# Kernel tuning notes

Measured on AMD Instinct MI355X. Metric: run time of the kernel, lower is better.

The kernel has to match this reference:

```python
import jax, jax.numpy as jnp
import numpy as np

D_MODEL = 768
NUM_HEADS = 12
HEAD_DIM = D_MODEL // NUM_HEADS


def setup_inputs() -> dict:
    key = jax.random.key(0)
    ks = jax.random.split(key, 9)
    B, S = 2, 2048
    s = 1.0 / np.sqrt(D_MODEL)
    x = jax.random.normal(ks[0], (B, S, D_MODEL), dtype=jnp.float32)
    Wq = jax.random.normal(ks[1], (D_MODEL, D_MODEL), dtype=jnp.float32) * s
    Wk = jax.random.normal(ks[2], (D_MODEL, D_MODEL), dtype=jnp.float32) * s
    Wv = jax.random.normal(ks[3], (D_MODEL, D_MODEL), dtype=jnp.float32) * s
    Wo = jax.random.normal(ks[4], (D_MODEL, D_MODEL), dtype=jnp.float32) * s
    bq = jax.random.normal(ks[5], (D_MODEL,), dtype=jnp.float32) * 0.01
    bk = jax.random.normal(ks[6], (D_MODEL,), dtype=jnp.float32) * 0.01
    bv = jax.random.normal(ks[7], (D_MODEL,), dtype=jnp.float32) * 0.01
    bo = jax.random.normal(ks[8], (D_MODEL,), dtype=jnp.float32) * 0.01
    return {"x": x, "Wq": Wq, "bq": bq, "Wk": Wk, "bk": bk,
            "Wv": Wv, "bv": bv, "Wo": Wo, "bo": bo}


def reference(x, Wq, bq, Wk, bk, Wv, bv, Wo, bo):
    B, S, _ = x.shape
    # projections; reshape to [B, H, S, Dh]
    def split_heads(t):
        return t.reshape(B, S, NUM_HEADS, HEAD_DIM).transpose(0, 2, 1, 3)
    q = split_heads(x @ Wq + bq)
    k = split_heads(x @ Wk + bk)
    v = split_heads(x @ Wv + bv)
    scale = 1.0 / np.sqrt(HEAD_DIM)
    scores = jnp.einsum("bhqd,bhkd->bhqk", q, k) * scale  # [B,H,S,S]
    attn = jax.nn.softmax(scores, axis=-1)
    # dropout p=0.0 (eval) -> identity
    ctx = jnp.einsum("bhqk,bhkd->bhqd", attn, v)
    ctx = ctx.transpose(0, 2, 1, 3).reshape(B, S, D_MODEL)
    return ctx @ Wo + bo
```

## Files before the change

kernel.cpp:

```cpp
#include <hip/hip_runtime.h>
#include <hip/hip_bf16.h>
#include <hip/hip_fp16.h>

#define D_MODEL 768
#define NHEADS  12
#define HD      64
#define BATCH   2
#define SEQ     2048
#define NTOK    (BATCH*SEQ)
#define NX      ((size_t)NTOK * D_MODEL)
#define NW      ((size_t)D_MODEL * D_MODEL)
#define SC_LOG2 0.18033688f

typedef __attribute__((ext_vector_type(8))) short    short8;
typedef __attribute__((ext_vector_type(8))) _Float16 half8;
typedef __attribute__((ext_vector_type(2))) __fp16   fp16x2;
typedef __attribute__((ext_vector_type(4))) float    f32x4;

__device__ __forceinline__ float bf2f(short s) {
    union { unsigned u; float f; } c;
    c.u = ((unsigned)(unsigned short)s) << 16;
    return c.f;
}
__device__ __forceinline__ short f2bf(float f) {
    __hip_bfloat16 h = __float2bfloat16(f);
    return *(short*)&h;
}

#ifdef __has_builtin
#if __has_builtin(__builtin_amdgcn_global_load_lds)
#define HAS_GLD 1
#endif
#if __has_builtin(__builtin_amdgcn_exp2f)
#define EXP2(x) __builtin_amdgcn_exp2f(x)
#else
#define EXP2(x) exp2f(x)
#endif
#if __has_builtin(__builtin_amdgcn_cvt_pkrtz)
#define HAS_PKRTZ 1
#endif
#else
#define EXP2(x) exp2f(x)
#endif
#ifdef HAS_GLD
#define GLD16(gp, lp) __builtin_amdgcn_global_load_lds( \
    (const __attribute__((address_space(1))) void*)(gp), \
    (__attribute__((address_space(3))) void*)(lp), 16, 0, 0)
#endif

__global__ __launch_bounds__(256) void fused_conv(
        const void* __restrict__ xin,
        const void* __restrict__ w0, const void* __restrict__ w1,
        const void* __restrict__ w2, const void* __restrict__ w3,
        const void* __restrict__ b0, const void* __restrict__ b1,
        const void* __restrict__ b2, const void* __restrict__ b3,
        short* __restrict__ xc, short* __restrict__ wt,
        short* __restrict__ bc, int* __restrict__ flag)
{
    __shared__ int red[256];
    __shared__ float T[64][65];
    const int tid = threadIdx.x;
    const int F = blockIdx.x;

    {
        const short* xs = (const short*)xin;
        int maxe = 0;
#pragma unroll
        for (int u = 0; u < 16; ++u) {
            int e = ((unsigned short)xs[tid * 16 + u] >> 7) & 0xFF;
            maxe = max(maxe, e);
        }
        red[tid] = maxe;
        __syncthreads();
        for (int s = 128; s > 0; s >>= 1) {
            if (tid < s) red[tid] = max(red[tid], red[tid + s]);
            __syncthreads();
        }
    }
    const bool isf = (red[0] > 140);

    if (F < 3072) {
        const int i = F * 256 + tid;
        if (isf) {
            float4 f = ((const float4*)xin)[i];
            short4 o = { f2bf(f.x), f2bf(f.y), f2bf(f.z), f2bf(f.w) };
            ((short4*)xc)[i] = o;
        } else {
            ((short4*)xc)[i] = ((const short4*)xin)[i];
        }
    } else if (F < 3648) {
        const int G = F - 3072;
        const int z = G / 144, rr = G % 144;
        const int k0 = (rr % 12) * 64, n0 = (rr / 12) * 64;
        const void* src = (z == 0) ? w0 : (z == 1) ? w1 : (z == 2) ? w2 : w3;
        const float sc = (z == 0) ? SC_LOG2 : 1.0f;
        const int la = tid & 15, lb = tid >> 4;
#pragma unroll
        for (int u = 0; u < 4; ++u) {
            const int kr = (lb & 3) + 4 * u + 16 * (lb >> 2);
            if (isf) {
                float4 f = *(const float4*)((const float*)src + (size_t)(k0 + kr) * D_MODEL + n0 + la * 4);
                T[kr][la*4+0] = f.x; T[kr][la*4+1] = f.y; T[kr][la*4+2] = f.z; T[kr][la*4+3] = f.w;
            } else {
                short4 s = *(const short4*)((const short*)src + (size_t)(k0 + kr) * D_MODEL + n0 + la * 4);
                T[kr][la*4+0] = bf2f(s.x); T[kr][la*4+1] = bf2f(s.y);
                T[kr][la*4+2] = bf2f(s.z); T[kr][la*4+3] = bf2f(s.w);
            }
        }
        __syncthreads();
#pragma unroll
        for (int u = 0; u < 4; ++u) {
            const int nr = (lb & 3) + 4 * u + 16 * (lb >> 2);
            short4 o = { f2bf(T[la*4+0][nr] * sc), f2bf(T[la*4+1][nr] * sc),
                         f2bf(T[la*4+2][nr] * sc), f2bf(T[la*4+3][nr] * sc) };
            *(short4*)(wt + (size_t)z * NW + (size_t)(n0 + nr) * D_MODEL + k0 + la * 4) = o;
        }
    } else {
        if (tid == 0) *flag = isf ? 1 : 0;
        const void* srcs[4] = { b0, b1, b2, b3 };
        for (int z = 0; z < 4; ++z) {
            const float sc = (z == 0) ? SC_LOG2 : 1.0f;
            for (int i = tid; i < D_MODEL; i += 256) {
                float v = isf ? ((const float*)srcs[z])[i] : bf2f(((const short*)srcs[z])[i]);
                bc[z * D_MODEL + i] = f2bf(v * sc);
            }
        }
    }
}

__global__ __launch_bounds__(256) void qkv_gemm(const short* __restrict__ X,
                                                const short* __restrict__ Wt,
                                                const short* __restrict__ bias,
                                                short* __restrict__ qb,
                                                short* __restrict__ kb,
                                                _Float16* __restrict__ Vt)
{
    __shared__ __align__(16) char shbuf[32768];
    short* Als = (short*)shbuf;
    short* Bls = (short*)(shbuf + 16384);
    _Float16* T = (_Float16*)shbuf;

    const int tid = threadIdx.x;
    const int wave = tid >> 6, lane = tid & 63;
    const int quad = lane >> 4, l16 = lane & 15;
    const int wm = wave & 1, wn = wave >> 1;
    const int m0 = blockIdx.x * 128;
    const int ng = blockIdx.y * 128;

    f32x4 acc[4][4];
#pragma unroll
    for (int nt = 0; nt < 4; ++nt) {
        const float bv = bf2f(bias[ng + wn*64 + nt*16 + l16]);
#pragma unroll
        for (int mt = 0; mt < 4; ++mt) acc[mt][nt] = (f32x4){bv, bv, bv, bv};
    }

    const int row = tid >> 2, ch = (tid & 3) * 8;
#ifdef HAS_GLD
#define QSTAGE(buf, k0) do { \
        GLD16(X  + (size_t)(m0 + row)      * D_MODEL + (k0) + ch, &Als[(buf)*4096 + tid*8]); \
        GLD16(X  + (size_t)(m0 + 64 + row) * D_MODEL + (k0) + ch, &Als[(buf)*4096 + 2048 + tid*8]); \
        GLD16(Wt + (size_t)(ng + row)      * D_MODEL + (k0) + ch, &Bls[(buf)*4096 + tid*8]); \
        GLD16(Wt + (size_t)(ng + 64 + row) * D_MODEL + (k0) + ch, &Bls[(buf)*4096 + 2048 + tid*8]); \
    } while (0)
#else
#define QSTAGE(buf, k0) do { \
        short8 r0 = *(const short8*)(X  + (size_t)(m0 + row)      * D_MODEL + (k0) + ch); \
        short8 r1 = *(const short8*)(X  + (size_t)(m0 + 64 + row) * D_MODEL + (k0) + ch); \
        short8 r2 = *(const short8*)(Wt + (size_t)(ng + row)      * D_MODEL + (k0) + ch); \
        short8 r3 = *(const short8*)(Wt + (size_t)(ng + 64 + row) * D_MODEL + (k0) + ch); \
        *(short8*)&Als[(buf)*4096 + tid*8] = r0;  *(short8*)&Als[(buf)*4096 + 2048 + tid*8] = r1; \
        *(short8*)&Bls[(buf)*4096 + tid*8] = r2;  *(short8*)&Bls[(buf)*4096 + 2048 + tid*8] = r3; \
    } while (0)
#endif

    QSTAGE(0, 0);
    __syncthreads();

    for (int ks = 0; ks < 24; ++ks) {
        const int cur = ks & 1;
        if (ks + 1 < 24) QSTAGE(cur ^ 1, (ks + 1) * 32);

        short8 a[4], b[4];
#pragma unroll
        for (int mt = 0; mt < 4; ++mt)
            a[mt] = *(const short8*)&Als[cur*4096 + (wm*64 + mt*16 + l16) * 32 + quad*8];
#pragma unroll
        for (int nt = 0; nt < 4; ++nt)
            b[nt] = *(const short8*)&Bls[cur*4096 + (wn*64 + nt*16 + l16) * 32 + quad*8];
#pragma unroll
        for (int mt = 0; mt < 4; ++mt)
#pragma unroll
        for (int nt = 0; nt < 4; ++nt)
            acc[mt][nt] = __builtin_amdgcn_mfma_f32_16x16x32_bf16(a[mt], b[nt], acc[mt][nt], 0, 0, 0);

        __syncthreads();
    }
#undef QSTAGE

    const int seg = blockIdx.y / 6;
    if (seg < 2) {
        short* out = seg ? kb : qb;
        const int nl = ng - seg * 768;
#pragma unroll
        for (int mt = 0; mt < 4; ++mt)
#pragma unroll
        for (int nt = 0; nt < 4; ++nt) {
            const int n = nl + wn*64 + nt*16 + l16;
#pragma unroll
            for (int r = 0; r < 4; ++r) {
                const int m = m0 + wm*64 + mt*16 + quad*4 + r;
                out[(size_t)m * D_MODEL + n] = f2bf(acc[mt][nt][r]);
            }
        }
    } else {
        const int batch = m0 >> 11, tokb = m0 & (SEQ - 1);
        for (int pass = 0; pass < 2; ++pass) {
            if (wn == pass) {
#pragma unroll
                for (int nt = 0; nt < 4; ++nt) {
                    const int dim_l = nt*16 + l16;
#pragma unroll
                    for (int mt = 0; mt < 4; ++mt) {
                        const int tok_l = wm*64 + mt*16 + quad*4;
                        union { _Float16 h4[4]; int2 v; } u;
#pragma unroll
                        for (int r = 0; r < 4; ++r) u.h4[r] = (_Float16)acc[mt][nt][r];
                        *(int2*)&T[dim_l * 136 + tok_l] = u.v;
                    }
                }
            }
            __syncthreads();
#pragma unroll
            for (int u = 0; u < 4; ++u) {
                const int slot = tid + u * 256;
                const int drow = slot >> 4, chk = slot & 15;
                int4 val = *(const int4*)&T[drow * 136 + chk * 8];
                const int dim_g = ng - 1536 + pass*64 + drow;
                const int h = dim_g >> 6, d = dim_g & 63;
                *(int4*)(Vt + ((size_t)(batch * NHEADS + h) * HD + d) * SEQ + tokb + chk*8) = val;
            }
            if (pass == 0) __syncthreads();
        }
    }
}

__global__ __launch_bounds__(256) void out_gemm(const short* __restrict__ X,
                                                const short* __restrict__ Wt,
                                                const short* __restrict__ bias,
                                                void* __restrict__ outv,
                                                const int* __restrict__ flag)
{
    __shared__ short Als[2][2048];
    __shared__ short Bls[2][2048];

    const int tid = threadIdx.x;
    const int wave = tid >> 6, lane = tid & 63;
    const int quad = lane >> 4, l16 = lane & 15;
    const int m0 = blockIdx.x * 64;
    const int n0 = blockIdx.y * 64;

    f32x4 acc[4];
#pragma unroll
    for (int nt = 0; nt < 4; ++nt) {
        const float bv = bf2f(bias[n0 + nt*16 + l16]);
        acc[nt] = (f32x4){bv, bv, bv, bv};
    }

    const int row = tid >> 2, ch = (tid & 3) * 8;
#ifdef HAS_GLD
#define OSTAGE(buf, k0) do { \
        GLD16(X  + (size_t)(m0 + row) * D_MODEL + (k0) + ch, &Als[buf][tid*8]); \
        GLD16(Wt + (size_t)(n0 + row) * D_MODEL + (k0) + ch, &Bls[buf][tid*8]); \
    } while (0)
#else
#define OSTAGE(buf, k0) do { \
        short8 r0 = *(const short8*)(X  + (size_t)(m0 + row) * D_MODEL + (k0) + ch); \
        short8 r1 = *(const short8*)(Wt + (size_t)(n0 + row) * D_MODEL + (k0) + ch); \
        *(short8*)&Als[buf][tid*8] = r0; \
        *(short8*)&Bls[buf][tid*8] = r1; \
    } while (0)
#endif

    OSTAGE(0, 0);
    __syncthreads();

    for (int ks = 0; ks < 24; ++ks) {
        const int cur = ks & 1;
        if (ks + 1 < 24) OSTAGE(cur ^ 1, (ks + 1) * 32);

        short8 a = *(const short8*)&Als[cur][(wave*16 + l16) * 32 + quad*8];
#pragma unroll
        for (int nt = 0; nt < 4; ++nt) {
            short8 b = *(const short8*)&Bls[cur][(nt*16 + l16) * 32 + quad*8];
            acc[nt] = __builtin_amdgcn_mfma_f32_16x16x32_bf16(a, b, acc[nt], 0, 0, 0);
        }
        __syncthreads();
    }
#undef OSTAGE

    const bool outf32 = (*flag != 0);
#pragma unroll
    for (int nt = 0; nt < 4; ++nt) {
        const int n = n0 + nt*16 + l16;
#pragma unroll
        for (int r = 0; r < 4; ++r) {
            const int m = m0 + wave*16 + quad*4 + r;
            const size_t idx = (size_t)m * D_MODEL + n;
            if (outf32) ((float*)outv)[idx] = acc[nt][r];
            else        ((short*)outv)[idx] = f2bf(acc[nt][r]);
        }
    }
}

__global__ __launch_bounds__(256) void attn_mfma(const short* __restrict__ q,
                                                 const short* __restrict__ k,
                                                 const _Float16* __restrict__ Vt,
                                                 short* __restrict__ ctx)
{
    __shared__ short    Kls[2][64 * 64];
    __shared__ _Float16 Vls[2][64 * 64];
    __shared__ _Float16 Pls[4][16 * 64];

    const int tid  = threadIdx.x;
    const int wave = tid >> 6, lane = tid & 63;
    const int quad = lane >> 4, l16 = lane & 15;

    const int F = blockIdx.x;
    const int xcd = F & 7, slot = F >> 3;
    const int bh = xcd * 3 + (slot >> 5);
    const int q0 = (slot & 31) * 64;
    const int b = bh / NHEADS, h = bh % NHEADS;
    const size_t bS = (size_t)b * SEQ;
    const int myq = q0 + wave * 16 + l16;

    short8 qf[2];
#pragma unroll
    for (int k0h = 0; k0h < 2; ++k0h)
        qf[k0h] = *(const short8*)(q + (bS + myq) * D_MODEL + h*HD + k0h*32 + quad*8);

    half8 ones;
#pragma unroll
    for (int j = 0; j < 8; ++j) ones[j] = (_Float16)1.0f;

    const int s0 = tid, s1 = tid + 256;
    const int kr0 = s0 >> 3, kc0 = (s0 & 7) ^ (kr0 & 7);
    const int kr1 = s1 >> 3, kc1 = (s1 & 7) ^ (kr1 & 7);
    const short*    kg0 = k  + (bS + kr0) * D_MODEL + h*HD + kc0*8;
    const short*    kg1 = k  + (bS + kr1) * D_MODEL + h*HD + kc1*8;
    const _Float16* vg0 = Vt + ((size_t)bh * HD + kr0) * SEQ + kc0*8;
    const _Float16* vg1 = Vt + ((size_t)bh * HD + kr1) * SEQ + kc1*8;

#ifdef HAS_GLD
#define STAGE(buf, j0) do { \
        GLD16(kg0 + (size_t)(j0) * D_MODEL, &Kls[buf][s0 * 8]); \
        GLD16(kg1 + (size_t)(j0) * D_MODEL, &Kls[buf][s1 * 8]); \
        GLD16(vg0 + (j0),                   &Vls[buf][s0 * 8]); \
        GLD16(vg1 + (j0),                   &Vls[buf][s1 * 8]); \
    } while (0)
#else
#define STAGE(buf, j0) do { \
        short8 a_ = *(const short8*)(kg0 + (size_t)(j0) * D_MODEL); \
        short8 b_ = *(const short8*)(kg1 + (size_t)(j0) * D_MODEL); \
        half8  c_ = *(const half8*)(vg0 + (j0)); \
        half8  d_ = *(const half8*)(vg1 + (j0)); \
        *(short8*)&Kls[buf][s0 * 8] = a_;  *(short8*)&Kls[buf][s1 * 8] = b_; \
        *(half8*)&Vls[buf][s0 * 8] = c_;   *(half8*)&Vls[buf][s1 * 8] = d_; \
    } while (0)
#endif

    float m_ = -1e30f;
    f32x4 lacc = (f32x4){0.f, 0.f, 0.f, 0.f};
    f32x4 o[4];
#pragma unroll
    for (int t = 0; t < 4; ++t) o[t] = (f32x4){0.f, 0.f, 0.f, 0.f};

    STAGE(0, 0);
    __syncthreads();

    for (int jt = 0; jt < SEQ / 64; ++jt) {
        const int cur = jt & 1;
        if (jt + 1 < SEQ / 64) STAGE(cur ^ 1, (jt + 1) * 64);

        f32x4 s4[4];
#pragma unroll
        for (int t = 0; t < 4; ++t) s4[t] = (f32x4){0.f, 0.f, 0.f, 0.f};
#pragma unroll
        for (int k0h = 0; k0h < 2; ++k0h)
#pragma unroll
        for (int t = 0; t < 4; ++t) {
            const int krow = t*16 + l16;
            short8 kf = *(const short8*)&Kls[cur][krow*64 + (((k0h*4 + quad) ^ (krow & 7)) * 8)];
            s4[t] = __builtin_amdgcn_mfma_f32_16x16x32_bf16(kf, qf[k0h], s4[t], 0, 0, 0);
        }

        float mx = s4[0][0];
#pragma unroll
        for (int t = 0; t < 4; ++t)
#pragma unroll
        for (int r = 0; r < 4; ++r) mx = fmaxf(mx, s4[t][r]);
        if (__any(mx > m_)) {
#pragma unroll
            for (int d = 1; d < 64; d <<= 1) mx = fmaxf(mx, __shfl_xor(mx, d));
            const float mn = fmaxf(m_, mx);
            const float al = EXP2(m_ - mn);
#pragma unroll
            for (int t = 0; t < 4; ++t) {
                o[t][0] *= al; o[t][1] *= al; o[t][2] *= al; o[t][3] *= al;
            }
            lacc[0] *= al; lacc[1] *= al; lacc[2] *= al; lacc[3] *= al;
            m_ = mn;
        }

#pragma unroll
        for (int t = 0; t < 4; ++t) {
            union { fp16x2 h2[2]; int2 v; } u4;
#ifdef HAS_PKRTZ
            u4.h2[0] = __builtin_amdgcn_cvt_pkrtz(EXP2(s4[t][0] - m_), EXP2(s4[t][1] - m_));
            u4.h2[1] = __builtin_amdgcn_cvt_pkrtz(EXP2(s4[t][2] - m_), EXP2(s4[t][3] - m_));
#else
            u4.h2[0] = (fp16x2){ (__fp16)EXP2(s4[t][0] - m_), (__fp16)EXP2(s4[t][1] - m_) };
            u4.h2[1] = (fp16x2){ (__fp16)EXP2(s4[t][2] - m_), (__fp16)EXP2(s4[t][3] - m_) };
#endif
            const int c = (t*2 + (quad >> 1)) ^ (l16 & 7);
            *(int2*)&Pls[wave][l16*64 + c*8 + (quad & 1)*4] = u4.v;
        }

#pragma unroll
        for (int k0h = 0; k0h < 2; ++k0h) {
            const int pc = (k0h*4 + quad) ^ (l16 & 7);
            half8 pf = *(half8*)&Pls[wave][l16*64 + pc*8];
            lacc = __builtin_amdgcn_mfma_f32_16x16x32_f16(ones, pf, lacc, 0, 0, 0);
#pragma unroll
            for (int t = 0; t < 4; ++t) {
                const int vrow = t*16 + l16;
                half8 vf = *(const half8*)&Vls[cur][vrow*64 + (((k0h*4 + quad) ^ (vrow & 7)) * 8)];
                o[t] = __builtin_amdgcn_mfma_f32_16x16x32_f16(vf, pf, o[t], 0, 0, 0);
            }
        }

        __syncthreads();
    }

    const float inv = 1.0f / lacc[0];
    const size_t rowp = (bS + myq) * D_MODEL + h*HD;
#pragma unroll
    for (int t = 0; t < 4; ++t) {
        union { short s4v[4]; int2 v; } u4;
#pragma unroll
        for (int r = 0; r < 4; ++r) u4.s4v[r] = f2bf(o[t][r] * inv);
        *(int2*)(ctx + rowp + t*16 + quad*4) = u4.v;
    }
#undef STAGE
}

extern "C" void kernel_launch(void* const* d_in, const int* in_sizes, int n_in,
                              void* d_out, int out_size, void* d_ws, size_t ws_size,
                              hipStream_t stream)
{
    int* flag = (int*)d_ws;
    short* xc = (short*)((char*)d_ws + 64);
    short* Wt = xc + NX;
    short* bc = Wt + 4 * NW;
    short* qb = bc + 4 * D_MODEL;
    short* kb = qb + NX;
    _Float16* Vt = (_Float16*)(kb + NX);
    short* cb = (short*)(Vt + NX);

    fused_conv<<<3649, 256, 0, stream>>>(d_in[0],
                                         d_in[1], d_in[3], d_in[5], d_in[7],
                                         d_in[2], d_in[4], d_in[6], d_in[8],
                                         xc, Wt, bc, flag);

    qkv_gemm<<<dim3(NTOK/128, 2304/128), 256, 0, stream>>>(xc, Wt, bc, qb, kb, Vt);

    attn_mfma<<<768, 256, 0, stream>>>(qb, kb, Vt, cb);

    out_gemm<<<dim3(NTOK/64, D_MODEL/64), 256, 0, stream>>>(cb, Wt + 3*NW, bc + 3*D_MODEL, d_out, flag);
}
```

Baseline: 182.4 us.

## Process two 16-row query groups per wave in attention, halving block threads

```diff
diff --git a/kernel.cpp b/kernel.cpp
--- a/kernel.cpp
+++ b/kernel.cpp
@@ -313,14 +313,14 @@
     }
 }
 
-__global__ __launch_bounds__(256) void attn_mfma(const short* __restrict__ q,
+__global__ __launch_bounds__(128) void attn_mfma(const short* __restrict__ q,
                                                  const short* __restrict__ k,
                                                  const _Float16* __restrict__ Vt,
                                                  short* __restrict__ ctx)
 {
     __shared__ short    Kls[2][64 * 64];
     __shared__ _Float16 Vls[2][64 * 64];
-    __shared__ _Float16 Pls[4][16 * 64];
+    __shared__ _Float16 Pls[2][32 * 64];
 
     const int tid  = threadIdx.x;
     const int wave = tid >> 6, lane = tid & 63;
@@ -332,48 +332,77 @@
     const int q0 = (slot & 31) * 64;
     const int b = bh / NHEADS, h = bh % NHEADS;
     const size_t bS = (size_t)b * SEQ;
-    const int myq = q0 + wave * 16 + l16;
-
-    short8 qf[2];
+    const int qbase = q0 + wave * 32;
+
+    short8 qf[2][2];
+#pragma unroll
+    for (int qg = 0; qg < 2; ++qg)
 #pragma unroll
     for (int k0h = 0; k0h < 2; ++k0h)
-        qf[k0h] = *(const short8*)(q + (bS + myq) * D_MODEL + h*HD + k0h*32 + quad*8);
+        qf[qg][k0h] = *(const short8*)(q + (bS + qbase + qg*16 + l16) * D_MODEL
+                                         + h*HD + k0h*32 + quad*8);
 
     half8 ones;
 #pragma unroll
     for (int j = 0; j < 8; ++j) ones[j] = (_Float16)1.0f;
 
-    const int s0 = tid, s1 = tid + 256;
-    const int kr0 = s0 >> 3, kc0 = (s0 & 7) ^ (kr0 & 7);
-    const int kr1 = s1 >> 3, kc1 = (s1 & 7) ^ (kr1 & 7);
-    const short*    kg0 = k  + (bS + kr0) * D_MODEL + h*HD + kc0*8;
-    const short*    kg1 = k  + (bS + kr1) * D_MODEL + h*HD + kc1*8;
-    const _Float16* vg0 = Vt + ((size_t)bh * HD + kr0) * SEQ + kc0*8;
-    const _Float16* vg1 = Vt + ((size_t)bh * HD + kr1) * SEQ + kc1*8;
+    int kr[4], kc[4];
+#pragma unroll
+    for (int u = 0; u < 4; ++u) {
+        const int s = tid + u * 128;
+        kr[u] = s >> 3;
+        kc[u] = (s & 7) ^ (kr[u] & 7);
+    }
+    const short*    kg0 = k  + (bS + kr[0]) * D_MODEL + h*HD + kc[0]*8;
+    const short*    kg1 = k  + (bS + kr[1]) * D_MODEL + h*HD + kc[1]*8;
+    const short*    kg2 = k  + (bS + kr[2]) * D_MODEL + h*HD + kc[2]*8;
+    const short*    kg3 = k  + (bS + kr[3]) * D_MODEL + h*HD + kc[3]*8;
+    const _Float16* vg0 = Vt + ((size_t)bh * HD + kr[0]) * SEQ + kc[0]*8;
+    const _Float16* vg1 = Vt + ((size_t)bh * HD + kr[1]) * SEQ + kc[1]*8;
+    const _Float16* vg2 = Vt + ((size_t)bh * HD + kr[2]) * SEQ + kc[2]*8;
+    const _Float16* vg3 = Vt + ((size_t)bh * HD + kr[3]) * SEQ + kc[3]*8;
 
 #ifdef HAS_GLD
 #define STAGE(buf, j0) do { \
-        GLD16(kg0 + (size_t)(j0) * D_MODEL, &Kls[buf][s0 * 8]); \
-        GLD16(kg1 + (size_t)(j0) * D_MODEL, &Kls[buf][s1 * 8]); \
-        GLD16(vg0 + (j0),                   &Vls[buf][s0 * 8]); \
-        GLD16(vg1 + (j0),                   &Vls[buf][s1 * 8]); \
+        GLD16(kg0 + (size_t)(j0) * D_MODEL, &Kls[buf][(tid      ) * 8]); \
+        GLD16(kg1 + (size_t)(j0) * D_MODEL, &Kls[buf][(tid + 128) * 8]); \
+        GLD16(kg2 + (size_t)(j0) * D_MODEL, &Kls[buf][(tid + 256) * 8]); \
+        GLD16(kg3 + (size_t)(j0) * D_MODEL, &Kls[buf][(tid + 384) * 8]); \
+        GLD16(vg0 + (j0),                   &Vls[buf][(tid      ) * 8]); \
+        GLD16(vg1 + (j0),                   &Vls[buf][(tid + 128) * 8]); \
+        GLD16(vg2 + (j0),                   &Vls[buf][(tid + 256) * 8]); \
+        GLD16(vg3 + (j0),                   &Vls[buf][(tid + 384) * 8]); \
     } while (0)
 #else
 #define STAGE(buf, j0) do { \
-        short8 a_ = *(const short8*)(kg0 + (size_t)(j0) * D_MODEL); \
-        short8 b_ = *(const short8*)(kg1 + (size_t)(j0) * D_MODEL); \
-        half8  c_ = *(const half8*)(vg0 + (j0)); \
-        half8  d_ = *(const half8*)(vg1 + (j0)); \
-        *(short8*)&Kls[buf][s0 * 8] = a_;  *(short8*)&Kls[buf][s1 * 8] = b_; \
-        *(half8*)&Vls[buf][s0 * 8] = c_;   *(half8*)&Vls[buf][s1 * 8] = d_; \
+        short8 a0_ = *(const short8*)(kg0 + (size_t)(j0) * D_MODEL); \
+        short8 a1_ = *(const short8*)(kg1 + (size_t)(j0) * D_MODEL); \
+        short8 a2_ = *(const short8*)(kg2 + (size_t)(j0) * D_MODEL); \
+        short8 a3_ = *(const short8*)(kg3 + (size_t)(j0) * D_MODEL); \
+        half8  c0_ = *(const half8*)(vg0 + (j0)); \
+        half8  c1_ = *(const half8*)(vg1 + (j0)); \
+        half8  c2_ = *(const half8*)(vg2 + (j0)); \
+        half8  c3_ = *(const half8*)(vg3 + (j0)); \
+        *(short8*)&Kls[buf][(tid      ) * 8] = a0_; \
+        *(short8*)&Kls[buf][(tid + 128) * 8] = a1_; \
+        *(short8*)&Kls[buf][(tid + 256) * 8] = a2_; \
+        *(short8*)&Kls[buf][(tid + 384) * 8] = a3_; \
+        *(half8*)&Vls[buf][(tid      ) * 8] = c0_; \
+        *(half8*)&Vls[buf][(tid + 128) * 8] = c1_; \
+        *(half8*)&Vls[buf][(tid + 256) * 8] = c2_; \
+        *(half8*)&Vls[buf][(tid + 384) * 8] = c3_; \
     } while (0)
 #endif
 
     float m_ = -1e30f;
-    f32x4 lacc = (f32x4){0.f, 0.f, 0.f, 0.f};
-    f32x4 o[4];
-#pragma unroll
-    for (int t = 0; t < 4; ++t) o[t] = (f32x4){0.f, 0.f, 0.f, 0.f};
+    f32x4 lacc[2];
+    f32x4 o[2][4];
+#pragma unroll
+    for (int qg = 0; qg < 2; ++qg) {
+        lacc[qg] = (f32x4){0.f, 0.f, 0.f, 0.f};
+#pragma unroll
+        for (int t = 0; t < 4; ++t) o[qg][t] = (f32x4){0.f, 0.f, 0.f, 0.f};
+    }
 
     STAGE(0, 0);
     __syncthreads();
@@ -382,74 +411,96 @@
         const int cur = jt & 1;
         if (jt + 1 < SEQ / 64) STAGE(cur ^ 1, (jt + 1) * 64);
 
-        f32x4 s4[4];
-#pragma unroll
-        for (int t = 0; t < 4; ++t) s4[t] = (f32x4){0.f, 0.f, 0.f, 0.f};
+        f32x4 s4[2][4];
+#pragma unroll
+        for (int qg = 0; qg < 2; ++qg)
+#pragma unroll
+        for (int t = 0; t < 4; ++t) s4[qg][t] = (f32x4){0.f, 0.f, 0.f, 0.f};
 #pragma unroll
         for (int k0h = 0; k0h < 2; ++k0h)
 #pragma unroll
         for (int t = 0; t < 4; ++t) {
             const int krow = t*16 + l16;
             short8 kf = *(const short8*)&Kls[cur][krow*64 + (((k0h*4 + quad) ^ (krow & 7)) * 8)];
-            s4[t] = __builtin_amdgcn_mfma_f32_16x16x32_bf16(kf, qf[k0h], s4[t], 0, 0, 0);
-        }
-
-        float mx = s4[0][0];
+#pragma unroll
+            for (int qg = 0; qg < 2; ++qg)
+                s4[qg][t] = __builtin_amdgcn_mfma_f32_16x16x32_bf16(kf, qf[qg][k0h], s4[qg][t], 0, 0, 0);
+        }
+
+        float mx = s4[0][0][0];
+#pragma unroll
+        for (int qg = 0; qg < 2; ++qg)
 #pragma unroll
         for (int t = 0; t < 4; ++t)
 #pragma unroll
-        for (int r = 0; r < 4; ++r) mx = fmaxf(mx, s4[t][r]);
+        for (int r = 0; r < 4; ++r) mx = fmaxf(mx, s4[qg][t][r]);
         if (__any(mx > m_)) {
 #pragma unroll
             for (int d = 1; d < 64; d <<= 1) mx = fmaxf(mx, __shfl_xor(mx, d));
             const float mn = fmaxf(m_, mx);
             const float al = EXP2(m_ - mn);
 #pragma unroll
-            for (int t = 0; t < 4; ++t) {
-                o[t][0] *= al; o[t][1] *= al; o[t][2] *= al; o[t][3] *= al;
-            }
-            lacc[0] *= al; lacc[1] *= al; lacc[2] *= al; lacc[3] *= al;
+            for (int qg = 0; qg < 2; ++qg) {
+#pragma unroll
+                for (int t = 0; t < 4; ++t) {
+                    o[qg][t][0] *= al; o[qg][t][1] *= al;
+                    o[qg][t][2] *= al; o[qg][t][3] *= al;
+                }
+                lacc[qg][0] *= al; lacc[qg][1] *= al;
+                lacc[qg][2] *= al; lacc[qg][3] *= al;
+            }
             m_ = mn;
         }
 
+#pragma unroll
+        for (int qg = 0; qg < 2; ++qg)
 #pragma unroll
         for (int t = 0; t < 4; ++t) {
             union { fp16x2 h2[2]; int2 v; } u4;
 #ifdef HAS_PKRTZ
-            u4.h2[0] = __builtin_amdgcn_cvt_pkrtz(EXP2(s4[t][0] - m_), EXP2(s4[t][1] - m_));
-            u4.h2[1] = __builtin_amdgcn_cvt_pkrtz(EXP2(s4[t][2] - m_), EXP2(s4[t][3] - m_));
+            u4.h2[0] = __builtin_amdgcn_cvt_pkrtz(EXP2(s4[qg][t][0] - m_), EXP2(s4[qg][t][1] - m_));
+            u4.h2[1] = __builtin_amdgcn_cvt_pkrtz(EXP2(s4[qg][t][2] - m_), EXP2(s4[qg][t][3] - m_));
 #else
-            u4.h2[0] = (fp16x2){ (__fp16)EXP2(s4[t][0] - m_), (__fp16)EXP2(s4[t][1] - m_) };
-            u4.h2[1] = (fp16x2){ (__fp16)EXP2(s4[t][2] - m_), (__fp16)EXP2(s4[t][3] - m_) };
+            u4.h2[0] = (fp16x2){ (__fp16)EXP2(s4[qg][t][0] - m_), (__fp16)EXP2(s4[qg][t][1] - m_) };
+            u4.h2[1] = (fp16x2){ (__fp16)EXP2(s4[qg][t][2] - m_), (__fp16)EXP2(s4[qg][t][3] - m_) };
 #endif
             const int c = (t*2 + (quad >> 1)) ^ (l16 & 7);
-            *(int2*)&Pls[wave][l16*64 + c*8 + (quad & 1)*4] = u4.v;
+            *(int2*)&Pls[wave][(qg*16 + l16)*64 + c*8 + (quad & 1)*4] = u4.v;
         }
 
 #pragma unroll
         for (int k0h = 0; k0h < 2; ++k0h) {
             const int pc = (k0h*4 + quad) ^ (l16 & 7);
-            half8 pf = *(half8*)&Pls[wave][l16*64 + pc*8];
-            lacc = __builtin_amdgcn_mfma_f32_16x16x32_f16(ones, pf, lacc, 0, 0, 0);
+            half8 pf[2];
+#pragma unroll
+            for (int qg = 0; qg < 2; ++qg) {
+                pf[qg] = *(half8*)&Pls[wave][(qg*16 + l16)*64 + pc*8];
+                lacc[qg] = __builtin_amdgcn_mfma_f32_16x16x32_f16(ones, pf[qg], lacc[qg], 0, 0, 0);
+            }
 #pragma unroll
             for (int t = 0; t < 4; ++t) {
                 const int vrow = t*16 + l16;
                 half8 vf = *(const half8*)&Vls[cur][vrow*64 + (((k0h*4 + quad) ^ (vrow & 7)) * 8)];
-                o[t] = __builtin_amdgcn_mfma_f32_16x16x32_f16(vf, pf, o[t], 0, 0, 0);
+#pragma unroll
+                for (int qg = 0; qg < 2; ++qg)
+                    o[qg][t] = __builtin_amdgcn_mfma_f32_16x16x32_f16(vf, pf[qg], o[qg][t], 0, 0, 0);
             }
         }
 
         __syncthreads();
     }
 
-    const float inv = 1.0f / lacc[0];
-    const size_t rowp = (bS + myq) * D_MODEL + h*HD;
-#pragma unroll
-    for (int t = 0; t < 4; ++t) {
-        union { short s4v[4]; int2 v; } u4;
-#pragma unroll
-        for (int r = 0; r < 4; ++r) u4.s4v[r] = f2bf(o[t][r] * inv);
-        *(int2*)(ctx + rowp + t*16 + quad*4) = u4.v;
+#pragma unroll
+    for (int qg = 0; qg < 2; ++qg) {
+        const float inv = 1.0f / lacc[qg][0];
+        const size_t rowp = (bS + qbase + qg*16 + l16) * D_MODEL + h*HD;
+#pragma unroll
+        for (int t = 0; t < 4; ++t) {
+            union { short s4v[4]; int2 v; } u4;
+#pragma unroll
+            for (int r = 0; r < 4; ++r) u4.s4v[r] = f2bf(o[qg][t][r] * inv);
+            *(int2*)(ctx + rowp + t*16 + quad*4) = u4.v;
+        }
     }
 #undef STAGE
 }
@@ -474,7 +525,7 @@
 
     qkv_gemm<<<dim3(NTOK/128, 2304/128), 256, 0, stream>>>(xc, Wt, bc, qb, kb, Vt);
 
-    attn_mfma<<<768, 256, 0, stream>>>(qb, kb, Vt, cb);
+    attn_mfma<<<768, 128, 0, stream>>>(qb, kb, Vt, cb);
 
     out_gemm<<<dim3(NTOK/64, D_MODEL/64), 256, 0, stream>>>(cb, Wt + 3*NW, bc + 3*D_MODEL, d_out, flag);
 }
```

Result: slower. 189.0 us (+3.6%).
